# Optimization experiments

Measured on AMD Instinct MI355X. Metric: run time of the kernel, lower is better.

Reference implementation:

```python
import jax, jax.numpy as jnp
import numpy as np

D_MODEL = 1024
NHEAD = 16
HEAD_DIM = D_MODEL // NHEAD
EPS = 1e-5


def _layer_norm(x, gamma, beta):
    mu = jnp.mean(x, axis=-1, keepdims=True)
    var = jnp.mean(jnp.square(x - mu), axis=-1, keepdims=True)
    return (x - mu) * jax.lax.rsqrt(var + EPS) * gamma + beta


def setup_inputs() -> dict:
    key = jax.random.key(0)
    ks = jax.random.split(key, 8)
    s = 1.0 / np.sqrt(D_MODEL)
    return {
        "x": jax.random.normal(ks[0], (4, 2048, D_MODEL), dtype=jnp.float32),
        "Wq": jax.random.uniform(ks[1], (D_MODEL, D_MODEL), jnp.float32, -s, s),
        "Wk": jax.random.uniform(ks[2], (D_MODEL, D_MODEL), jnp.float32, -s, s),
        "Wv": jax.random.uniform(ks[3], (D_MODEL, D_MODEL), jnp.float32, -s, s),
        "ln1_g": jnp.ones((D_MODEL,), jnp.float32),
        "ln1_b": jnp.zeros((D_MODEL,), jnp.float32),
        "ln2_g": jnp.ones((D_MODEL,), jnp.float32),
        "ln2_b": jnp.zeros((D_MODEL,), jnp.float32),
        "W1": jax.random.uniform(ks[4], (D_MODEL, D_MODEL), jnp.float32, -s, s),
        "b1": jax.random.uniform(ks[5], (D_MODEL,), jnp.float32, -s, s),
        "W2": jax.random.uniform(ks[6], (D_MODEL, D_MODEL), jnp.float32, -s, s),
        "b2": jax.random.uniform(ks[7], (D_MODEL,), jnp.float32, -s, s),
    }


def reference(x, Wq, Wk, Wv, ln1_g, ln1_b, ln2_g, ln2_b, W1, b1, W2, b2):
    B, S, D = x.shape
    temperature = jnp.sqrt(jnp.asarray(D_MODEL / NHEAD, x.dtype))
    xn = _layer_norm(x, ln1_g, ln1_b)
    # torch Linear: y = x @ W.T (weights are [out, in], no bias for q/k/v)
    q = (xn @ Wq.T).reshape(B, S, NHEAD, HEAD_DIM)
    k = (xn @ Wk.T).reshape(B, S, NHEAD, HEAD_DIM)
    v = (xn @ Wv.T).reshape(B, S, NHEAD, HEAD_DIM)
    scores = jnp.einsum("bqhd,bkhd->bhqk", q, k) / temperature  # [B,H,S,S]
    causal = jnp.tril(jnp.ones((S, S), dtype=bool))
    scores = jnp.where(causal, scores, jnp.asarray(-jnp.inf, scores.dtype))
    attn = jax.nn.softmax(scores, axis=-1)
    att_out = jnp.einsum("bhqk,bkhd->bqhd", attn, v).reshape(B, S, D)
    xt = x + att_out
    xt2 = _layer_norm(xt, ln2_g, ln2_b)
    ffn = jax.nn.relu(xt2 @ W1.T + b1) @ W2.T + b2  # dropout=0 -> identity
    return xt + ffn
```

## Files before the change

kernel.cpp:

```cpp
#include <hip/hip_runtime.h>
#include <hip/hip_bf16.h>

typedef unsigned short u16;
typedef unsigned int u32;
typedef __attribute__((ext_vector_type(8))) __bf16 bf16x8;
typedef __attribute__((ext_vector_type(4))) float f32x4;
typedef __attribute__((ext_vector_type(16))) float f32x16;
typedef __attribute__((ext_vector_type(8))) unsigned short ushort8v;
typedef __attribute__((ext_vector_type(4))) unsigned short u16x4;
typedef __attribute__((ext_vector_type(4))) unsigned int u32x4;

#define DEV __device__ __forceinline__
#define AS1 __attribute__((address_space(1)))
#define AS3 __attribute__((address_space(3)))

DEV u16 f2bf(float f) {
    union { float f; unsigned int i; } u; u.f = f;
    unsigned int x = u.i;
    unsigned int r = (x + 0x7fffu + ((x >> 16) & 1u)) >> 16;
    return (u16)r;
}
DEV float bf2f(u16 h) {
    union { unsigned int i; float f; } u; u.i = ((unsigned int)h) << 16;
    return u.f;
}
DEV u32 cvt_pk_bf16(float lo, float hi) {
    u32 r;
    asm("v_cvt_pk_bf16_f32 %0, %1, %2" : "=v"(r) : "v"(lo), "v"(hi));
    return r;
}
DEV void pl32swap(u32& a, u32& b) {
    asm volatile("v_permlane32_swap_b32 %0, %1" : "+v"(a), "+v"(b));
}

__global__ __launch_bounds__(256) void ln1_cvt(
    const float* __restrict__ xin,
    const float* __restrict__ g, const float* __restrict__ be,
    u16* __restrict__ y_bf,
    const float* __restrict__ wq, const float* __restrict__ wk,
    const float* __restrict__ wv, const float* __restrict__ w1,
    const float* __restrict__ w2, u16* __restrict__ wdst)
{
    const int tid = threadIdx.x;
    if (blockIdx.x >= 8192) {
        const int i = ((blockIdx.x - 8192) * 256 + tid) * 4;
        auto conv4 = [](float4 a) {
            u16x4 r; r[0] = f2bf(a.x); r[1] = f2bf(a.y); r[2] = f2bf(a.z); r[3] = f2bf(a.w);
            return r;
        };
        *(u16x4*)(wdst + i)               = conv4(*(const float4*)(wq + i));
        *(u16x4*)(wdst + (1 << 20) + i)   = conv4(*(const float4*)(wk + i));
        *(u16x4*)(wdst + (2 << 20) + i)   = conv4(*(const float4*)(wv + i));
        *(u16x4*)(wdst + (3 << 20) + i)   = conv4(*(const float4*)(w1 + i));
        *(u16x4*)(wdst + (4 << 20) + i)   = conv4(*(const float4*)(w2 + i));
        return;
    }
    const int row = blockIdx.x;
    const size_t base = (size_t)row * 1024 + tid * 4;
    float4 xv = *(const float4*)(xin + base);
    float v[4] = {xv.x, xv.y, xv.z, xv.w};
    float s = 0.f, ss = 0.f;
    #pragma unroll
    for (int j = 0; j < 4; ++j) { s += v[j]; ss += v[j] * v[j]; }
    #pragma unroll
    for (int o = 32; o > 0; o >>= 1) { s += __shfl_xor(s, o); ss += __shfl_xor(ss, o); }
    __shared__ float red[8];
    const int w = tid >> 6;
    if ((tid & 63) == 0) { red[w * 2] = s; red[w * 2 + 1] = ss; }
    __syncthreads();
    s  = red[0] + red[2] + red[4] + red[6];
    ss = red[1] + red[3] + red[5] + red[7];
    const float mu = s * (1.0f / 1024.0f);
    const float var = ss * (1.0f / 1024.0f) - mu * mu;
    const float rstd = rsqrtf(var + 1e-5f);
    const int col = tid * 4;
    float4 gv = *(const float4*)(g + col);
    float4 bv = *(const float4*)(be + col);
    u16x4 o4;
    o4[0] = f2bf((v[0] - mu) * rstd * gv.x + bv.x);
    o4[1] = f2bf((v[1] - mu) * rstd * gv.y + bv.y);
    o4[2] = f2bf((v[2] - mu) * rstd * gv.z + bv.z);
    o4[3] = f2bf((v[3] - mu) * rstd * gv.w + bv.w);
    *(u16x4*)(y_bf + base) = o4;
}

__global__ __launch_bounds__(256) void ln2_kernel(
    const float* __restrict__ xin, const u16* __restrict__ addbf,
    const float* __restrict__ g, const float* __restrict__ be,
    u16* __restrict__ xt_out, u16* __restrict__ y_bf)
{
    const int row = blockIdx.x;
    const int tid = threadIdx.x;
    const size_t base = (size_t)row * 1024 + tid * 4;

    float4 xv = *(const float4*)(xin + base);
    float v[4] = {xv.x, xv.y, xv.z, xv.w};
    u16x4 a = *(const u16x4*)(addbf + base);
    v[0] += bf2f(a[0]); v[1] += bf2f(a[1]); v[2] += bf2f(a[2]); v[3] += bf2f(a[3]);
    u16x4 o;
    o[0] = f2bf(v[0]); o[1] = f2bf(v[1]); o[2] = f2bf(v[2]); o[3] = f2bf(v[3]);
    *(u16x4*)(xt_out + base) = o;

    float s = 0.f, ss = 0.f;
    #pragma unroll
    for (int j = 0; j < 4; ++j) { s += v[j]; ss += v[j] * v[j]; }
    #pragma unroll
    for (int o2 = 32; o2 > 0; o2 >>= 1) { s += __shfl_xor(s, o2); ss += __shfl_xor(ss, o2); }
    __shared__ float red[8];
    const int w = tid >> 6;
    if ((tid & 63) == 0) { red[w * 2] = s; red[w * 2 + 1] = ss; }
    __syncthreads();
    s  = red[0] + red[2] + red[4] + red[6];
    ss = red[1] + red[3] + red[5] + red[7];
    const float mu = s * (1.0f / 1024.0f);
    const float var = ss * (1.0f / 1024.0f) - mu * mu;
    const float rstd = rsqrtf(var + 1e-5f);

    const int col = tid * 4;
    float4 gv = *(const float4*)(g + col);
    float4 bv = *(const float4*)(be + col);
    u16x4 o4;
    o4[0] = f2bf((v[0] - mu) * rstd * gv.x + bv.x);
    o4[1] = f2bf((v[1] - mu) * rstd * gv.y + bv.y);
    o4[2] = f2bf((v[2] - mu) * rstd * gv.z + bv.z);
    o4[3] = f2bf((v[3] - mu) * rstd * gv.w + bv.w);
    *(u16x4*)(y_bf + base) = o4;
}

template<int EPI>
__global__ __launch_bounds__(256, 4) void gemm_bt(
    const u16* __restrict__ A, const u16* __restrict__ Bt,
    void* __restrict__ Cout, const float* __restrict__ bias,
    const u16* __restrict__ resid, int M, int N, int K)
{
    __shared__ u16 As[2 * 128 * 32];
    __shared__ u16 Bs[2 * 128 * 32];
    const int tid = threadIdx.x;
    const int l = tid & 63;
    const int w = tid >> 6;
    const int wm = w >> 1, wn = w & 1;
    const int fr = l & 15, fc = l >> 4;
    const size_t rowA0 = (size_t)blockIdx.x * 128;
    const size_t rowB0 = (size_t)blockIdx.y * 128;

    f32x4 acc[4][4] = {};
    const int ldoff = fr * 32 + fc * 8;

    const int nkt = K >> 6;
    for (int kt = 0; kt < nkt; ++kt) {
        __syncthreads();
        const int k0 = kt << 6;
        #pragma unroll
        for (int q = 0; q < 4; ++q) {
            const int row = (q & 1) * 64 + w * 16 + (l >> 2);
            const int kk  = (q >> 1) * 32 + (l & 3) * 8;
            const u16* ga = A  + (rowA0 + row) * K + k0 + kk;
            const u16* gb = Bt + (rowB0 + row) * K + k0 + kk;
            u16* da = As + q * 2048 + w * 512;
            u16* db = Bs + q * 2048 + w * 512;
            __builtin_amdgcn_global_load_lds((const AS1 void*)ga, (AS3 void*)da, 16, 0, 0);
            __builtin_amdgcn_global_load_lds((const AS1 void*)gb, (AS3 void*)db, 16, 0, 0);
        }
        __syncthreads();
        #pragma unroll
        for (int ks = 0; ks < 2; ++ks) {
            const u16* as_p = As + ks * 4096;
            const u16* bs_p = Bs + ks * 4096;
            bf16x8 af[4], bfv[4];
            #pragma unroll
            for (int m = 0; m < 4; ++m)
                af[m] = *(const bf16x8*)(as_p + (wm * 64 + m * 16) * 32 + ldoff);
            #pragma unroll
            for (int n = 0; n < 4; ++n)
                bfv[n] = *(const bf16x8*)(bs_p + (wn * 64 + n * 16) * 32 + ldoff);
            #pragma unroll
            for (int m = 0; m < 4; ++m)
                #pragma unroll
                for (int n = 0; n < 4; ++n)
                    acc[m][n] = __builtin_amdgcn_mfma_f32_16x16x32_bf16(
                        af[m], bfv[n], acc[m][n], 0, 0, 0);
        }
    }

    const int r0 = (int)rowA0 + wm * 64;
    const int c0 = (int)rowB0 + wn * 64;
    #pragma unroll
    for (int m = 0; m < 4; ++m) {
        #pragma unroll
        for (int n = 0; n < 4; ++n) {
            const int rowbase = r0 + m * 16 + fc * 4;
            const int col = c0 + n * 16 + fr;
            if constexpr (EPI == 0) {
                const int which = col >> 10;
                const int hh = (col >> 6) & 15;
                const int dd = col & 63;
                const size_t hb2 = (size_t)(rowbase >> 11) * 16 + hh;
                const int s0 = rowbase & 2047;
                if (which == 2) {
                    u16x4 pk;
                    #pragma unroll
                    for (int j = 0; j < 4; ++j) pk[j] = f2bf(acc[m][n][j]);
                    *(u16x4*)((u16*)Cout + (size_t)2 * 8388608 +
                              (hb2 * 64 + dd) * 2048 + s0) = pk;
                } else {
                    #pragma unroll
                    for (int j = 0; j < 4; ++j)
                        ((u16*)Cout)[(size_t)which * 8388608 +
                                     (hb2 * 2048 + s0 + j) * 64 + dd] =
                            f2bf(acc[m][n][j]);
                }
            } else {
                #pragma unroll
                for (int j = 0; j < 4; ++j) {
                    float v = acc[m][n][j];
                    const size_t idx = (size_t)(rowbase + j) * N + col;
                    if constexpr (EPI == 1) {
                        v += bias[col];
                        v = fmaxf(v, 0.0f);
                        ((u16*)Cout)[idx] = f2bf(v);
                    } else {
                        v += bias[col] + bf2f(resid[idx]);
                        ((float*)Cout)[idx] = v;
                    }
                }
            }
        }
    }
}

__global__ __launch_bounds__(128, 2) void attn_fwd(
    const u16* __restrict__ Qh, const u16* __restrict__ Kh,
    const u16* __restrict__ Vh, u16* __restrict__ attout)
{
    __shared__ u16 Ks[2][64 * 64];
    __shared__ u16 Vt[2][64 * 64];

    const int bid = blockIdx.x;
    const int pair = (bid >> 3) & 15;
    const int g = (bid & 7) + 8 * (bid >> 7);
    const int h = g & 15, b = g >> 4;

    const int tid = threadIdx.x, l = tid & 63, w = tid >> 6;
    const int lq = l & 31;
    const int hi = l >> 5;
    const int hi8 = hi * 8;
    const int hb = b * 16 + h;
    const size_t head = (size_t)hb << 17;
    const u16* kb_g = Kh + head;
    const u16* vb_g = Vh + head;

    const int swr = (lq & 7) << 3;

    const int grow0 = w * 32 + (l >> 3);
    const int gsw   = ((l & 7) * 8) ^ ((l >> 3) << 3);

    const float qs = 0.125f * 1.44269504f;

    #pragma unroll 1
    for (int half = 0; half < 2; ++half) {
        const int qt = half ? 31 - pair : pair;
        const int qbase = qt * 64 + w * 32;
        const int qg = qbase + lq;

        bf16x8 qf[4];
        {
            const u16* qp = Qh + head + (size_t)(qbase + lq) * 64 + hi8;
            #pragma unroll
            for (int ds = 0; ds < 4; ++ds) {
                qf[ds] = *(const bf16x8*)(qp + ds * 16);
                #pragma unroll
                for (int j = 0; j < 8; ++j)
                    qf[ds][j] = (__bf16)((float)qf[ds][j] * qs);
            }
        }

        f32x16 acc[2] = {};
        float l_part = 0.0f;

        const int nkt = qt + 1;
        int cur = 0;

        #pragma unroll
        for (int i = 0; i < 4; ++i) {
            const int row = grow0 + i * 8;
            __builtin_amdgcn_global_load_lds(
                (const AS1 void*)(kb_g + (size_t)row * 64 + gsw),
                (AS3 void*)(&Ks[0][0] + (w * 32 + i * 8) * 64), 16, 0, 0);
            __builtin_amdgcn_global_load_lds(
                (const AS1 void*)(vb_g + (size_t)row * 2048 + gsw),
                (AS3 void*)(&Vt[0][0] + (w * 32 + i * 8) * 64), 16, 0, 0);
        }
        __builtin_amdgcn_sched_barrier(0);
        asm volatile("s_waitcnt vmcnt(0)" ::: "memory");
        __builtin_amdgcn_s_barrier();

        #pragma unroll 1
        for (int kt = 0; kt < nkt; ++kt) {
            const int kv0 = kt * 64;
            const bool diag = (kt == qt);
            const u16* ksc = &Ks[cur][0];
            const u16* vtc = &Vt[cur][0];

            if (kt + 1 < nkt) {
                u16* ksn = &Ks[cur ^ 1][0];
                u16* vtn = &Vt[cur ^ 1][0];
                #pragma unroll
                for (int i = 0; i < 4; ++i) {
                    const int row = grow0 + i * 8;
                    __builtin_amdgcn_global_load_lds(
                        (const AS1 void*)(kb_g + (size_t)(kv0 + 64 + row) * 64 + gsw),
                        (AS3 void*)(ksn + (w * 32 + i * 8) * 64), 16, 0, 0);
                    __builtin_amdgcn_global_load_lds(
                        (const AS1 void*)(vb_g + (size_t)row * 2048 + kv0 + 64 + gsw),
                        (AS3 void*)(vtn + (w * 32 + i * 8) * 64), 16, 0, 0);
                }
            }
            __builtin_amdgcn_sched_barrier(0);

            auto do_kvblk = [&](int kvblk) {
                f32x16 sa = {};
                const u16* kbase = ksc + (lq + kvblk * 32) * 64;
                __builtin_amdgcn_s_setprio(1);
                #pragma unroll
                for (int ds = 0; ds < 4; ++ds) {
                    const bf16x8 kf = *(const bf16x8*)(kbase + ((ds * 16 + hi8) ^ swr));
                    sa = __builtin_amdgcn_mfma_f32_32x32x16_bf16(kf, qf[ds], sa, 0, 0, 0);
                }
                __builtin_amdgcn_s_setprio(0);

                if (diag) {
                    const int kvb = kv0 + kvblk * 32 + 4 * hi;
                    #pragma unroll
                    for (int r = 0; r < 16; ++r) {
                        const int kg = kvb + (r & 3) + 8 * (r >> 2);
                        if (kg > qg) sa[r] = -3.0e38f;
                    }
                }

                float ls = 0.0f;
                #pragma unroll
                for (int r = 0; r < 16; ++r) { sa[r] = exp2f(sa[r]); ls += sa[r]; }
                l_part += ls;

                u32 P0 = cvt_pk_bf16(sa[0],  sa[1]);
                u32 P1 = cvt_pk_bf16(sa[2],  sa[3]);
                u32 P2 = cvt_pk_bf16(sa[4],  sa[5]);
                u32 P3 = cvt_pk_bf16(sa[6],  sa[7]);
                u32 P4 = cvt_pk_bf16(sa[8],  sa[9]);
                u32 P5 = cvt_pk_bf16(sa[10], sa[11]);
                u32 P6 = cvt_pk_bf16(sa[12], sa[13]);
                u32 P7 = cvt_pk_bf16(sa[14], sa[15]);
                pl32swap(P0, P2); pl32swap(P1, P3);
                pl32swap(P4, P6); pl32swap(P5, P7);
                u32x4 w0 = {P0, P1, P2, P3};
                u32x4 w1 = {P4, P5, P6, P7};
                const bf16x8 pf0 = __builtin_bit_cast(bf16x8, w0);
                const bf16x8 pf1 = __builtin_bit_cast(bf16x8, w1);

                __builtin_amdgcn_s_setprio(1);
                #pragma unroll
                for (int dblk = 0; dblk < 2; ++dblk) {
                    const u16* vbase = vtc + (lq + dblk * 32) * 64;
                    const bf16x8 vf0 = *(const bf16x8*)(vbase + ((kvblk * 32 + hi8) ^ swr));
                    acc[dblk] = __builtin_amdgcn_mfma_f32_32x32x16_bf16(
                        vf0, pf0, acc[dblk], 0, 0, 0);
                    const bf16x8 vf1 = *(const bf16x8*)(vbase + ((kvblk * 32 + 16 + hi8) ^ swr));
                    acc[dblk] = __builtin_amdgcn_mfma_f32_32x32x16_bf16(
                        vf1, pf1, acc[dblk], 0, 0, 0);
                }
                __builtin_amdgcn_s_setprio(0);
            };

            do_kvblk(0);
            if (!(diag && w == 0))
                do_kvblk(1);

            __builtin_amdgcn_sched_barrier(0);
            asm volatile("s_waitcnt vmcnt(0)" ::: "memory");
            asm volatile("s_waitcnt lgkmcnt(0)" ::: "memory");
            __builtin_amdgcn_s_barrier();
            cur ^= 1;
        }

        const float l_tot = l_part + __shfl_xor(l_part, 32);
        const float inv = 1.0f / l_tot;
        const size_t obase = ((size_t)b * 2048 + qbase + lq) * 1024 + h * 64;
        #pragma unroll
        for (int dblk = 0; dblk < 2; ++dblk) {
            #pragma unroll
            for (int gq = 0; gq < 4; ++gq) {
                u16x4 o;
                #pragma unroll
                for (int j = 0; j < 4; ++j)
                    o[j] = f2bf(acc[dblk][4 * gq + j] * inv);
                *(u16x4*)(attout + obase + dblk * 32 + gq * 8 + 4 * hi) = o;
            }
        }
    }
}

extern "C" void kernel_launch(void* const* d_in, const int* in_sizes, int n_in,
                              void* d_out, int out_size, void* d_ws, size_t ws_size,
                              hipStream_t stream)
{
    const float* x    = (const float*)d_in[0];
    const float* Wq   = (const float*)d_in[1];
    const float* Wk   = (const float*)d_in[2];
    const float* Wv   = (const float*)d_in[3];
    const float* ln1g = (const float*)d_in[4];
    const float* ln1b = (const float*)d_in[5];
    const float* ln2g = (const float*)d_in[6];
    const float* ln2b = (const float*)d_in[7];
    const float* W1   = (const float*)d_in[8];
    const float* b1   = (const float*)d_in[9];
    const float* W2   = (const float*)d_in[10];
    const float* b2   = (const float*)d_in[11];

    char* ws = (char*)d_ws;
    u16*   wbf  = (u16*)(ws);
    u16*   xn   = (u16*)(ws + 10485760);
    u16*   qkvb = (u16*)(ws + 27262976);
    u16*   attb = (u16*)(ws + 77594624);
    u16*   xt   = (u16*)(ws + 94371840);

    ln1_cvt<<<9216, 256, 0, stream>>>(x, ln1g, ln1b, xn, Wq, Wk, Wv, W1, W2, wbf);
    gemm_bt<0><<<dim3(64, 24), 256, 0, stream>>>(xn, wbf, qkvb, nullptr, nullptr,
                                                 8192, 3072, 1024);
    attn_fwd<<<1024, 128, 0, stream>>>(qkvb, qkvb + 8388608, qkvb + 16777216, attb);
    ln2_kernel<<<8192, 256, 0, stream>>>(x, attb, ln2g, ln2b, xt, xn);
    gemm_bt<1><<<dim3(64, 8), 256, 0, stream>>>(xn, wbf + (3 << 20), qkvb, b1, nullptr,
                                                8192, 1024, 1024);
    gemm_bt<2><<<dim3(64, 8), 256, 0, stream>>>(qkvb, wbf + (4 << 20), d_out, b2, xt,
                                                8192, 1024, 1024);
}
```

Before: 227.0 us.

## Split attention KV blocks across four waves and fold Q scale into Wq

```diff
diff --git a/kernel.cpp b/kernel.cpp
--- a/kernel.cpp
+++ b/kernel.cpp
@@ -44,15 +44,17 @@
     const int tid = threadIdx.x;
     if (blockIdx.x >= 8192) {
         const int i = ((blockIdx.x - 8192) * 256 + tid) * 4;
-        auto conv4 = [](float4 a) {
-            u16x4 r; r[0] = f2bf(a.x); r[1] = f2bf(a.y); r[2] = f2bf(a.z); r[3] = f2bf(a.w);
+        auto conv4 = [](float4 a, float s) {
+            u16x4 r; r[0] = f2bf(a.x * s); r[1] = f2bf(a.y * s);
+            r[2] = f2bf(a.z * s); r[3] = f2bf(a.w * s);
             return r;
         };
-        *(u16x4*)(wdst + i)               = conv4(*(const float4*)(wq + i));
-        *(u16x4*)(wdst + (1 << 20) + i)   = conv4(*(const float4*)(wk + i));
-        *(u16x4*)(wdst + (2 << 20) + i)   = conv4(*(const float4*)(wv + i));
-        *(u16x4*)(wdst + (3 << 20) + i)   = conv4(*(const float4*)(w1 + i));
-        *(u16x4*)(wdst + (4 << 20) + i)   = conv4(*(const float4*)(w2 + i));
+        const float qs = 0.125f * 1.44269504f;
+        *(u16x4*)(wdst + i)               = conv4(*(const float4*)(wq + i), qs);
+        *(u16x4*)(wdst + (1 << 20) + i)   = conv4(*(const float4*)(wk + i), 1.0f);
+        *(u16x4*)(wdst + (2 << 20) + i)   = conv4(*(const float4*)(wv + i), 1.0f);
+        *(u16x4*)(wdst + (3 << 20) + i)   = conv4(*(const float4*)(w1 + i), 1.0f);
+        *(u16x4*)(wdst + (4 << 20) + i)   = conv4(*(const float4*)(w2 + i), 1.0f);
         return;
     }
     const int row = blockIdx.x;
@@ -228,7 +230,7 @@
     }
 }
 
-__global__ __launch_bounds__(128, 2) void attn_fwd(
+__global__ __launch_bounds__(256, 4) void attn_fwd(
     const u16* __restrict__ Qh, const u16* __restrict__ Kh,
     const u16* __restrict__ Vh, u16* __restrict__ attout)
 {
@@ -241,9 +243,9 @@
     const int h = g & 15, b = g >> 4;
 
     const int tid = threadIdx.x, l = tid & 63, w = tid >> 6;
-    const int lq = l & 31;
-    const int hi = l >> 5;
-    const int hi8 = hi * 8;
+    const int lq = l & 31, hi = l >> 5, hi8 = hi * 8;
+    const int qhalf = w & 1, kvblk = w >> 1;
+    const int kvb32 = kvblk * 32;
     const int hb = b * 16 + h;
     const size_t head = (size_t)hb << 17;
     const u16* kb_g = Kh + head;
@@ -251,27 +253,21 @@
 
     const int swr = (lq & 7) << 3;
 
-    const int grow0 = w * 32 + (l >> 3);
+    const int grow0 = w * 16 + (l >> 3);
     const int gsw   = ((l & 7) * 8) ^ ((l >> 3) << 3);
-
-    const float qs = 0.125f * 1.44269504f;
 
     #pragma unroll 1
     for (int half = 0; half < 2; ++half) {
         const int qt = half ? 31 - pair : pair;
-        const int qbase = qt * 64 + w * 32;
-        const int qg = qbase + lq;
+        const int qbw = qt * 64 + qhalf * 32;
+        const int qg = qbw + lq;
 
         bf16x8 qf[4];
         {
-            const u16* qp = Qh + head + (size_t)(qbase + lq) * 64 + hi8;
-            #pragma unroll
-            for (int ds = 0; ds < 4; ++ds) {
+            const u16* qp = Qh + head + (size_t)(qbw + lq) * 64 + hi8;
+            #pragma unroll
+            for (int ds = 0; ds < 4; ++ds)
                 qf[ds] = *(const bf16x8*)(qp + ds * 16);
-                #pragma unroll
-                for (int j = 0; j < 8; ++j)
-                    qf[ds][j] = (__bf16)((float)qf[ds][j] * qs);
-            }
         }
 
         f32x16 acc[2] = {};
@@ -281,14 +277,14 @@
         int cur = 0;
 
         #pragma unroll
-        for (int i = 0; i < 4; ++i) {
+        for (int i = 0; i < 2; ++i) {
             const int row = grow0 + i * 8;
             __builtin_amdgcn_global_load_lds(
                 (const AS1 void*)(kb_g + (size_t)row * 64 + gsw),
-                (AS3 void*)(&Ks[0][0] + (w * 32 + i * 8) * 64), 16, 0, 0);
+                (AS3 void*)(&Ks[0][0] + (w * 16 + i * 8) * 64), 16, 0, 0);
             __builtin_amdgcn_global_load_lds(
                 (const AS1 void*)(vb_g + (size_t)row * 2048 + gsw),
-                (AS3 void*)(&Vt[0][0] + (w * 32 + i * 8) * 64), 16, 0, 0);
+                (AS3 void*)(&Vt[0][0] + (w * 16 + i * 8) * 64), 16, 0, 0);
         }
         __builtin_amdgcn_sched_barrier(0);
         asm volatile("s_waitcnt vmcnt(0)" ::: "memory");
@@ -305,21 +301,21 @@
                 u16* ksn = &Ks[cur ^ 1][0];
                 u16* vtn = &Vt[cur ^ 1][0];
                 #pragma unroll
-                for (int i = 0; i < 4; ++i) {
+                for (int i = 0; i < 2; ++i) {
                     const int row = grow0 + i * 8;
                     __builtin_amdgcn_global_load_lds(
                         (const AS1 void*)(kb_g + (size_t)(kv0 + 64 + row) * 64 + gsw),
-                        (AS3 void*)(ksn + (w * 32 + i * 8) * 64), 16, 0, 0);
+                        (AS3 void*)(ksn + (w * 16 + i * 8) * 64), 16, 0, 0);
                     __builtin_amdgcn_global_load_lds(
                         (const AS1 void*)(vb_g + (size_t)row * 2048 + kv0 + 64 + gsw),
-                        (AS3 void*)(vtn + (w * 32 + i * 8) * 64), 16, 0, 0);
+                        (AS3 void*)(vtn + (w * 16 + i * 8) * 64), 16, 0, 0);
                 }
             }
             __builtin_amdgcn_sched_barrier(0);
 
-            auto do_kvblk = [&](int kvblk) {
+            if (!(diag && qhalf == 0 && kvblk == 1)) {
                 f32x16 sa = {};
-                const u16* kbase = ksc + (lq + kvblk * 32) * 64;
+                const u16* kbase = ksc + (kvb32 + lq) * 64;
                 __builtin_amdgcn_s_setprio(1);
                 #pragma unroll
                 for (int ds = 0; ds < 4; ++ds) {
@@ -328,11 +324,11 @@
                 }
                 __builtin_amdgcn_s_setprio(0);
 
-                if (diag) {
-                    const int kvb = kv0 + kvblk * 32 + 4 * hi;
+                if (diag && kvblk == qhalf) {
+                    const int kvbase = kv0 + kvb32 + 4 * hi;
                     #pragma unroll
                     for (int r = 0; r < 16; ++r) {
-                        const int kg = kvb + (r & 3) + 8 * (r >> 2);
+                        const int kg = kvbase + (r & 3) + 8 * (r >> 2);
                         if (kg > qg) sa[r] = -3.0e38f;
                     }
                 }
@@ -352,28 +348,24 @@
                 u32 P7 = cvt_pk_bf16(sa[14], sa[15]);
                 pl32swap(P0, P2); pl32swap(P1, P3);
                 pl32swap(P4, P6); pl32swap(P5, P7);
-                u32x4 w0 = {P0, P1, P2, P3};
-                u32x4 w1 = {P4, P5, P6, P7};
-                const bf16x8 pf0 = __builtin_bit_cast(bf16x8, w0);
-                const bf16x8 pf1 = __builtin_bit_cast(bf16x8, w1);
+                u32x4 w0v = {P0, P1, P2, P3};
+                u32x4 w1v = {P4, P5, P6, P7};
+                const bf16x8 pf0 = __builtin_bit_cast(bf16x8, w0v);
+                const bf16x8 pf1 = __builtin_bit_cast(bf16x8, w1v);
 
                 __builtin_amdgcn_s_setprio(1);
                 #pragma unroll
                 for (int dblk = 0; dblk < 2; ++dblk) {
                     const u16* vbase = vtc + (lq + dblk * 32) * 64;
-                    const bf16x8 vf0 = *(const bf16x8*)(vbase + ((kvblk * 32 + hi8) ^ swr));
+                    const bf16x8 vf0 = *(const bf16x8*)(vbase + ((kvb32 + hi8) ^ swr));
                     acc[dblk] = __builtin_amdgcn_mfma_f32_32x32x16_bf16(
                         vf0, pf0, acc[dblk], 0, 0, 0);
-                    const bf16x8 vf1 = *(const bf16x8*)(vbase + ((kvblk * 32 + 16 + hi8) ^ swr));
+                    const bf16x8 vf1 = *(const bf16x8*)(vbase + ((kvb32 + 16 + hi8) ^ swr));
                     acc[dblk] = __builtin_amdgcn_mfma_f32_32x32x16_bf16(
                         vf1, pf1, acc[dblk], 0, 0, 0);
                 }
                 __builtin_amdgcn_s_setprio(0);
-            };
-
-            do_kvblk(0);
-            if (!(diag && w == 0))
-                do_kvblk(1);
+            }
 
             __builtin_amdgcn_sched_barrier(0);
             asm volatile("s_waitcnt vmcnt(0)" ::: "memory");
@@ -382,20 +374,42 @@
             cur ^= 1;
         }
 
-        const float l_tot = l_part + __shfl_xor(l_part, 32);
-        const float inv = 1.0f / l_tot;
-        const size_t obase = ((size_t)b * 2048 + qbase + lq) * 1024 + h * 64;
-        #pragma unroll
-        for (int dblk = 0; dblk < 2; ++dblk) {
-            #pragma unroll
-            for (int gq = 0; gq < 4; ++gq) {
-                u16x4 o;
-                #pragma unroll
-                for (int j = 0; j < 4; ++j)
-                    o[j] = f2bf(acc[dblk][4 * gq + j] * inv);
-                *(u16x4*)(attout + obase + dblk * 32 + gq * 8 + 4 * hi) = o;
-            }
-        }
+        float* accs = (float*)&Ks[0][0];
+        float* lsh  = (float*)&Vt[0][0];
+        if (kvblk == 1) {
+            float* rgn = accs + qhalf * 2048;
+            #pragma unroll
+            for (int e = 0; e < 16; ++e) {
+                rgn[e * 64 + l]        = acc[0][e];
+                rgn[(16 + e) * 64 + l] = acc[1][e];
+            }
+            lsh[qhalf * 64 + l] = l_part;
+        }
+        __syncthreads();
+        if (kvblk == 0) {
+            const float* rgn = accs + qhalf * 2048;
+            #pragma unroll
+            for (int e = 0; e < 16; ++e) {
+                acc[0][e] += rgn[e * 64 + l];
+                acc[1][e] += rgn[(16 + e) * 64 + l];
+            }
+            l_part += lsh[qhalf * 64 + l];
+            const float l_tot = l_part + __shfl_xor(l_part, 32);
+            const float inv = 1.0f / l_tot;
+            const size_t obase = ((size_t)b * 2048 + qbw + lq) * 1024 + h * 64;
+            #pragma unroll
+            for (int dblk = 0; dblk < 2; ++dblk) {
+                #pragma unroll
+                for (int gq = 0; gq < 4; ++gq) {
+                    u16x4 o;
+                    #pragma unroll
+                    for (int j = 0; j < 4; ++j)
+                        o[j] = f2bf(acc[dblk][4 * gq + j] * inv);
+                    *(u16x4*)(attout + obase + dblk * 32 + gq * 8 + 4 * hi) = o;
+                }
+            }
+        }
+        __syncthreads();
     }
 }
 
@@ -426,7 +440,7 @@
     ln1_cvt<<<9216, 256, 0, stream>>>(x, ln1g, ln1b, xn, Wq, Wk, Wv, W1, W2, wbf);
     gemm_bt<0><<<dim3(64, 24), 256, 0, stream>>>(xn, wbf, qkvb, nullptr, nullptr,
                                                  8192, 3072, 1024);
-    attn_fwd<<<1024, 128, 0, stream>>>(qkvb, qkvb + 8388608, qkvb + 16777216, attb);
+    attn_fwd<<<1024, 256, 0, stream>>>(qkvb, qkvb + 8388608, qkvb + 16777216, attb);
     ln2_kernel<<<8192, 256, 0, stream>>>(x, attb, ln2g, ln2b, xt, xn);
     gemm_bt<1><<<dim3(64, 8), 256, 0, stream>>>(xn, wbf + (3 << 20), qkvb, b1, nullptr,
                                                 8192, 1024, 1024);
```

Measured after the change: 208.0 us (median of 3 runs). -8.4%, faster.
